# Kernel optimization log

Measured on AMD Instinct MI355X. Metric: run time of the kernel, lower is better.

The kernel has to match this reference:

```python
import jax, jax.numpy as jnp
import numpy as np
from jax import lax

B, T, F, H, L = 64, 2048, 128, 128, 2


def _lstm_layer(x, Wih, Whh, bih, bhh, h0, c0):
    """Single LSTM layer, torch gate order (i,f,g,o). x: [B,T,in] -> y: [B,T,H], hT, cT."""
    b = bih + bhh

    def step(carry, xt):
        h, c = carry
        gates = xt @ Wih.T + h @ Whh.T + b  # [B,4H]
        i, f, g, o = jnp.split(gates, 4, axis=-1)
        i = jax.nn.sigmoid(i)
        f = jax.nn.sigmoid(f)
        g = jnp.tanh(g)
        o = jax.nn.sigmoid(o)
        c = f * c + i * g
        h = o * jnp.tanh(c)
        return (h, c), h

    xs = jnp.swapaxes(x, 0, 1)  # [T,B,in]
    (hT, cT), ys = lax.scan(step, (h0, c0), xs)
    return jnp.swapaxes(ys, 0, 1), hT, cT


def setup_inputs() -> dict:
    key = jax.random.key(0)
    ks = jax.random.split(key, 20)
    s = 1.0 / np.sqrt(H)
    u = lambda k, shape: jax.random.uniform(k, shape, jnp.float32, -s, s)
    inp = {"x": jax.random.normal(ks[0], (B, T, F), jnp.float32)}
    i = 1
    for pre, in0 in (("enc", F), ("dec", H)):
        for l in range(L):
            d_in = in0 if l == 0 else H
            inp[f"{pre}_Wih{l}"] = u(ks[i], (4 * H, d_in)); i += 1
            inp[f"{pre}_Whh{l}"] = u(ks[i], (4 * H, H)); i += 1
            inp[f"{pre}_bih{l}"] = u(ks[i], (4 * H,)); i += 1
            inp[f"{pre}_bhh{l}"] = u(ks[i], (4 * H,)); i += 1
    inp["out_W"] = u(ks[i], (F, H)); i += 1
    inp["out_b"] = u(ks[i], (F,))
    return inp


def reference(x,
              enc_Wih0, enc_Whh0, enc_bih0, enc_bhh0,
              enc_Wih1, enc_Whh1, enc_bih1, enc_bhh1,
              dec_Wih0, dec_Whh0, dec_bih0, dec_bhh0,
              dec_Wih1, dec_Whh1, dec_bih1, dec_bhh1,
              out_W, out_b):
    z = jnp.zeros((x.shape[0], H), x.dtype)
    # encoder: 2 stacked layers, zero initial state
    y0, h0, c0 = _lstm_layer(x, enc_Wih0, enc_Whh0, enc_bih0, enc_bhh0, z, z)
    y1, h1, c1 = _lstm_layer(y0, enc_Wih1, enc_Whh1, enc_bih1, enc_bhh1, z, z)
    # decoder: zeros input, initial state = encoder final (h,c) per layer
    dec_in = jnp.zeros_like(x)  # valid since n_features == hidden_dim
    d0, _, _ = _lstm_layer(dec_in, dec_Wih0, dec_Whh0, dec_bih0, dec_bhh0, h0, c0)
    d1, _, _ = _lstm_layer(d0, dec_Wih1, dec_Whh1, dec_bih1, dec_bhh1, h1, c1)
    return d1 @ out_W.T + out_b
```

## Files before the change

### kernel.cpp

```cpp
#include <hip/hip_runtime.h>
#include <cstdint>
#include <cstddef>

typedef float    float4v __attribute__((ext_vector_type(4)));
typedef _Float16 f16x4   __attribute__((ext_vector_type(4)));
typedef _Float16 f16x8   __attribute__((ext_vector_type(8)));
typedef unsigned long long u64;
struct u64p { u64 a, b; };

#define DI __device__ __forceinline__

static const int Bsz = 64, Tlen = 2048, Hd = 128, G4 = 512;
static const int HSTR = 144;
static const int RING = 256;
static const int YSTR = 136;

DI float sigf_fast(float x) {
    float e = __builtin_amdgcn_exp2f(-1.442695041f * x);
    return __builtin_amdgcn_rcpf(1.f + e);
}
DI float tanhf_fast(float x) {
    float e = __builtin_amdgcn_exp2f(-2.885390082f * x);
    return 2.f * __builtin_amdgcn_rcpf(1.f + e) - 1.f;
}

DI void lds_barrier() {
    asm volatile("s_waitcnt lgkmcnt(0)\n\ts_barrier" ::: "memory");
}

DI void pin(f16x8& v) {
    float4v t = __builtin_bit_cast(float4v, v);
    asm volatile("" : "+v"(t));
    v = __builtin_bit_cast(f16x8, t);
}

DI f16x8 cvt8(const float* p) {
    float4v u = *(const float4v*)p;
    float4v w = *(const float4v*)(p + 4);
    f16x8 o;
    o[0] = (_Float16)u[0]; o[1] = (_Float16)u[1]; o[2] = (_Float16)u[2]; o[3] = (_Float16)u[3];
    o[4] = (_Float16)w[0]; o[5] = (_Float16)w[1]; o[6] = (_Float16)w[2]; o[7] = (_Float16)w[3];
    return o;
}

DI u64 pack4(float4v a) {
    f16x4 h;
    h[0] = (_Float16)a[0]; h[1] = (_Float16)a[1];
    h[2] = (_Float16)a[2]; h[3] = (_Float16)a[3];
    return __builtin_bit_cast(u64, h);
}

DI u64 ald64(const void* pp) {
    return __hip_atomic_load((const u64*)pp, __ATOMIC_RELAXED, __HIP_MEMORY_SCOPE_AGENT);
}
DI void ast64(void* pp, u64 v) {
    __hip_atomic_store((u64*)pp, v, __ATOMIC_RELAXED, __HIP_MEMORY_SCOPE_AGENT);
}
DI void ast16(void* pp, unsigned short v) {
    __hip_atomic_store((unsigned short*)pp, v, __ATOMIC_RELAXED, __HIP_MEMORY_SCOPE_AGENT);
}
DI unsigned int aldu32(const unsigned int* pp) {
    return __hip_atomic_load(pp, __ATOMIC_RELAXED, __HIP_MEMORY_SCOPE_AGENT);
}
DI void astu32(unsigned int* pp, unsigned int v) {
    __hip_atomic_store(pp, v, __ATOMIC_RELAXED, __HIP_MEMORY_SCOPE_AGENT);
}

template <bool P_HAS_XP, bool P_INIT, bool C_INIT, bool R3_OUT>
__global__ __launch_bounds__(512, 1) void lstm_fused5(
    const float* __restrict__ Up, const float* __restrict__ bip, const float* __restrict__ bhp,
    const float* __restrict__ php, const float* __restrict__ pcp,
    float* __restrict__ fhp, float* __restrict__ fcp,
    const float* __restrict__ Wc, const float* __restrict__ Uc,
    const float* __restrict__ bic, const float* __restrict__ bhc,
    const float* __restrict__ phc, const float* __restrict__ pcc,
    float* __restrict__ fhc, float* __restrict__ fcc,
    const float* __restrict__ Wx, const float* __restrict__ xin,
    const float* __restrict__ oW, const float* __restrict__ ob,
    float* __restrict__ outp,
    _Float16* __restrict__ PB,
    _Float16* __restrict__ X2,
    _Float16* __restrict__ X1,
    _Float16* __restrict__ Y1,
    unsigned int* __restrict__ prog,  unsigned int* __restrict__ prog2,
    unsigned int* __restrict__ prog3, unsigned int* __restrict__ prog4,
    unsigned int* __restrict__ prog5, int T)
{
    const int tid  = threadIdx.x;
    const int lane = tid & 63, w = tid >> 6;
    const int col  = lane & 15, quad = lane >> 4;
    const int b    = col & 3, s = col >> 2;
    const int role = blockIdx.x >> 4;
    const int p    = blockIdx.x & 15;
    const int bglob = p * 4 + b;
    const int j    = w * 16 + s * 4 + quad;
    const int NG   = T >> 3;

    __shared__ alignas(16) _Float16 Hl[2 * 4 * HSTR];
    __shared__ alignas(16) _Float16 Ylh[32 * YSTR];

    unsigned int* pr  = prog  + p * 16;
    unsigned int* pr2 = prog2 + p * 16;
    unsigned int* pr3 = P_HAS_XP ? prog3 + p * 16 : nullptr;
    unsigned int* pr4 = R3_OUT   ? prog4 + p * 16 : nullptr;
    unsigned int* pr5 = R3_OUT   ? prog5 + p * 16 : nullptr;

    if (role == 0) {
        f16x8 af[4][4];
#pragma unroll
        for (int mt = 0; mt < 4; mt++) {
            int urow = (col & 3) * 128 + (w * 16 + mt * 4 + (col >> 2));
            const float* ur = Up + (size_t)urow * 128;
#pragma unroll
            for (int kc = 0; kc < 4; kc++) af[mt][kc] = cvt8(ur + kc * 32 + quad * 8);
        }
#pragma unroll
        for (int mt = 0; mt < 4; mt++)
#pragma unroll
            for (int kc = 0; kc < 4; kc++) pin(af[mt][kc]);

        float bq[4];
#pragma unroll
        for (int q = 0; q < 4; q++) bq[q] = bip[q * 128 + j] + bhp[q * 128 + j];

        float c = 0.f, hv = 0.f;
        if (P_INIT) {
            c  = pcp[(size_t)bglob * 128 + j];
            hv = php[(size_t)bglob * 128 + j];
        }
        Hl[b * HSTR + j] = (_Float16)hv;
        __syncthreads();

        const _Float16* x1b = P_HAS_XP ? X1 + (size_t)bglob * RING * 512 + 4 * j : nullptr;
        unsigned short* pbp = (unsigned short*)PB + (size_t)bglob * RING * 128 + j;

        if constexpr (P_HAS_XP) {
            if (tid == 511) {
                unsigned int need = 16u; if (need > (unsigned int)T) need = (unsigned int)T;
                unsigned int psn = aldu32(pr3);
                while (psn < need) { __builtin_amdgcn_s_sleep(8); psn = aldu32(pr3); }
            }
            __syncthreads();
        }
        f16x4 xp = {};
        if (P_HAS_XP) xp = __builtin_bit_cast(f16x4, ald64(x1b));

        int cur = 0;
        for (int g = 0; g < NG; g++) {
#pragma unroll
            for (int k = 0; k < 8; k++) {
                const int t = g * 8 + k;
                f16x4 xpn = {};
                if (P_HAS_XP)
                    xpn = __builtin_bit_cast(f16x4, ald64(x1b + (size_t)((t + 1) & (RING - 1)) * 512));

                const _Float16* Hc = Hl + cur * (4 * HSTR);
                f16x8 bf[4];
#pragma unroll
                for (int kc = 0; kc < 4; kc++)
                    bf[kc] = *(const f16x8*)(Hc + b * HSTR + kc * 32 + quad * 8);

                float4v acc[4] = {};
#pragma unroll
                for (int kc = 0; kc < 4; kc++)
#pragma unroll
                    for (int mt = 0; mt < 4; mt++)
                        acc[mt] = __builtin_amdgcn_mfma_f32_16x16x32_f16(af[mt][kc], bf[kc], acc[mt], 0, 0, 0);

                float4v t0 = (s & 1) ? acc[1] : acc[0];
                float4v t1 = (s & 1) ? acc[3] : acc[2];
                float4v gg = (s & 2) ? t1 : t0;

                float g0 = gg[0] + bq[0], g1 = gg[1] + bq[1], g2 = gg[2] + bq[2], g3 = gg[3] + bq[3];
                if (P_HAS_XP) { g0 += (float)xp[0]; g1 += (float)xp[1]; g2 += (float)xp[2]; g3 += (float)xp[3]; }
                float iv = sigf_fast(g0), fv = sigf_fast(g1);
                float gv = tanhf_fast(g2), ov = sigf_fast(g3);
                c  = fv * c + iv * gv;
                hv = ov * tanhf_fast(c);

                _Float16 hf = (_Float16)hv;
                Hl[(cur ^ 1) * (4 * HSTR) + b * HSTR + j] = hf;
                ast16(pbp + (size_t)(t & (RING - 1)) * 128,
                      __builtin_bit_cast(unsigned short, hf));

                if (k == 7) {
                    if constexpr (P_HAS_XP) asm volatile("s_waitcnt vmcnt(2)" ::: "memory");
                    else                    asm volatile("s_waitcnt vmcnt(1)" ::: "memory");
                    if (tid == 0) astu32(pr, (unsigned int)(g * 8 + 7));
                    if constexpr (P_HAS_XP) {
                        if (tid == 511 && g + 1 < NG) {
                            unsigned int need = (unsigned int)(8 * (g + 1) + 16);
                            if (need > (unsigned int)T) need = (unsigned int)T;
                            unsigned int psn = aldu32(pr3);
                            while (psn < need) { __builtin_amdgcn_s_sleep(2); psn = aldu32(pr3); }
                        }
                    }
                }
                lds_barrier();
                xp = xpn;
                cur ^= 1;
            }
        }

        asm volatile("s_waitcnt vmcnt(0)" ::: "memory");
        __syncthreads();
        if (tid == 0) astu32(pr, (unsigned int)T);

        fhp[(size_t)bglob * 128 + j] = hv;
        fcp[(size_t)bglob * 128 + j] = c;
    } else if (role == 1) {
        f16x8 afH[4][4];
#pragma unroll
        for (int mt = 0; mt < 4; mt++) {
            int urow = (col & 3) * 128 + (w * 16 + mt * 4 + (col >> 2));
            const float* ur = Uc + (size_t)urow * 128;
#pragma unroll
            for (int kc = 0; kc < 4; kc++) afH[mt][kc] = cvt8(ur + kc * 32 + quad * 8);
        }
#pragma unroll
        for (int mt = 0; mt < 4; mt++)
#pragma unroll
            for (int kc = 0; kc < 4; kc++) pin(afH[mt][kc]);

        float bq[4];
#pragma unroll
        for (int q = 0; q < 4; q++) bq[q] = bic[q * 128 + j] + bhc[q * 128 + j];

        float c = 0.f, hv = 0.f;
        if (C_INIT) {
            c  = pcc[(size_t)bglob * 128 + j];
            hv = phc[(size_t)bglob * 128 + j];
        }
        Hl[b * HSTR + j] = (_Float16)hv;

        if (tid == 511) {
            unsigned int need = 9u; if (need > (unsigned int)T) need = (unsigned int)T;
            unsigned int psn = aldu32(pr2);
            while (psn < need) { __builtin_amdgcn_s_sleep(8); psn = aldu32(pr2); }
        }
        __syncthreads();

        const _Float16* x2b = X2 + (size_t)bglob * RING * 512 + 4 * j;
        unsigned short* y1p = R3_OUT ? (unsigned short*)Y1 + (size_t)bglob * RING * 128 + j : nullptr;
        f16x4 xp = __builtin_bit_cast(f16x4, ald64(x2b));

        int cur = 0;
        for (int g = 0; g < NG; g++) {
#pragma unroll
            for (int k = 0; k < 8; k++) {
                const int t = g * 8 + k;
                const int slot = (t + 1) & (RING - 1);
                f16x4 xpn = __builtin_bit_cast(f16x4, ald64(x2b + (size_t)slot * 512));

                const _Float16* Hc = Hl + cur * (4 * HSTR);
                f16x8 bf[4];
#pragma unroll
                for (int kc = 0; kc < 4; kc++)
                    bf[kc] = *(const f16x8*)(Hc + b * HSTR + kc * 32 + quad * 8);

                float4v acc[4] = {};
#pragma unroll
                for (int kc = 0; kc < 4; kc++)
#pragma unroll
                    for (int mt = 0; mt < 4; mt++)
                        acc[mt] = __builtin_amdgcn_mfma_f32_16x16x32_f16(afH[mt][kc], bf[kc], acc[mt], 0, 0, 0);

                float4v t0 = (s & 1) ? acc[1] : acc[0];
                float4v t1 = (s & 1) ? acc[3] : acc[2];
                float4v gg = (s & 2) ? t1 : t0;

                float g0 = gg[0] + bq[0] + (float)xp[0], g1 = gg[1] + bq[1] + (float)xp[1];
                float g2 = gg[2] + bq[2] + (float)xp[2], g3 = gg[3] + bq[3] + (float)xp[3];
                float iv = sigf_fast(g0), fv = sigf_fast(g1);
                float gv = tanhf_fast(g2), ov = sigf_fast(g3);
                c  = fv * c + iv * gv;
                hv = ov * tanhf_fast(c);

                _Float16 hf = (_Float16)hv;
                Hl[(cur ^ 1) * (4 * HSTR) + b * HSTR + j] = hf;
                if constexpr (R3_OUT)
                    ast16(y1p + (size_t)(t & (RING - 1)) * 128,
                          __builtin_bit_cast(unsigned short, hf));

                if (k == 7) {
                    if constexpr (R3_OUT) {
                        asm volatile("s_waitcnt vmcnt(2)" ::: "memory");
                        if (tid == 0) astu32(pr4, (unsigned int)(g * 8 + 7));
                    }
                    if (tid == 511 && g + 1 < NG) {
                        unsigned int need = (unsigned int)(8 * (g + 1) + 9);
                        if (need > (unsigned int)T) need = (unsigned int)T;
                        unsigned int psn = aldu32(pr2);
                        while (psn < need) { __builtin_amdgcn_s_sleep(2); psn = aldu32(pr2); }
                        if constexpr (R3_OUT) {
                            if (g + 1 >= 32) {
                                unsigned int need5 = (unsigned int)(8 * (g + 1 - 32) + 8);
                                unsigned int p5 = aldu32(pr5);
                                while (p5 < need5) { __builtin_amdgcn_s_sleep(2); p5 = aldu32(pr5); }
                            }
                        }
                    }
                }
                lds_barrier();
                xp = xpn;
                cur ^= 1;
            }
        }

        if constexpr (R3_OUT) {
            asm volatile("s_waitcnt vmcnt(0)" ::: "memory");
            __syncthreads();
            if (tid == 0) astu32(pr4, (unsigned int)T);
        }
        fhc[(size_t)bglob * 128 + j] = hv;
        fcc[(size_t)bglob * 128 + j] = c;
    } else if (role == 2) {
        f16x8 bw[4][4];
#pragma unroll
        for (int nt = 0; nt < 4; nt++) {
            int n = (w * 4 + nt) * 16 + col;
            int wrow = (n & 3) * 128 + (n >> 2);
            const float* Wr = Wc + (size_t)wrow * 128;
#pragma unroll
            for (int kc = 0; kc < 4; kc++) bw[nt][kc] = cvt8(Wr + kc * 32 + quad * 8);
        }
#pragma unroll
        for (int nt = 0; nt < 4; nt++)
#pragma unroll
            for (int kc = 0; kc < 4; kc++) pin(bw[nt][kc]);

        const int lrow = tid >> 4, lchunk = tid & 15;
        const int lb = lrow & 3, ltr = lrow >> 2;

        for (int g = 0; g < NG; g++) {
            if (tid == 0) {
                unsigned int need = (unsigned int)(g * 8 + 8);
                unsigned int psn = aldu32(pr);
                while (psn < need) { __builtin_amdgcn_s_sleep(4); psn = aldu32(pr); }
            }
            __syncthreads();
            {
                int slot = (g * 8 + ltr) & (RING - 1);
                const char* srcp = (const char*)(PB + ((size_t)(p * 4 + lb) * RING + slot) * 128 + lchunk * 8);
                u64 a0 = ald64(srcp);
                u64 a1 = ald64(srcp + 8);
                char* dst = (char*)&Ylh[lrow * YSTR + lchunk * 8];
                *(u64*)dst = a0;
                *(u64*)(dst + 8) = a1;
            }
            lds_barrier();

            float4v acc[2][4] = {};
#pragma unroll
            for (int kc = 0; kc < 4; kc++) {
                f16x8 y0 = *(const f16x8*)&Ylh[col * YSTR + kc * 32 + quad * 8];
                f16x8 y1t = *(const f16x8*)&Ylh[(16 + col) * YSTR + kc * 32 + quad * 8];
#pragma unroll
                for (int nt = 0; nt < 4; nt++) {
                    acc[0][nt] = __builtin_amdgcn_mfma_f32_16x16x32_f16(bw[nt][kc], y0,  acc[0][nt], 0, 0, 0);
                    acc[1][nt] = __builtin_amdgcn_mfma_f32_16x16x32_f16(bw[nt][kc], y1t, acc[1][nt], 0, 0, 0);
                }
            }
            {
                const int bb = col & 3;
#pragma unroll
                for (int mt = 0; mt < 2; mt++) {
                    int trow = mt * 4 + (col >> 2);
                    int slot = (g * 8 + trow) & (RING - 1);
                    _Float16* dst = X2 + ((size_t)(p * 4 + bb) * RING + slot) * 512 + (w * 4) * 16 + quad * 4;
#pragma unroll
                    for (int nt = 0; nt < 4; nt++)
                        ast64(dst + nt * 16, pack4(acc[mt][nt]));
                }
            }
            asm volatile("s_waitcnt vmcnt(0)" ::: "memory");
            __syncthreads();
            if (tid == 0) astu32(pr2, (unsigned int)(g * 8 + 8));
        }
    } else if constexpr (!R3_OUT) {
        f16x8 bw[4][4];
#pragma unroll
        for (int nt = 0; nt < 4; nt++) {
            int n = (w * 4 + nt) * 16 + col;
            int wrow = (n & 3) * 128 + (n >> 2);
            const float* Wr = Wx + (size_t)wrow * 128;
#pragma unroll
            for (int kc = 0; kc < 4; kc++) bw[nt][kc] = cvt8(Wr + kc * 32 + quad * 8);
        }
#pragma unroll
        for (int nt = 0; nt < 4; nt++)
#pragma unroll
            for (int kc = 0; kc < 4; kc++) pin(bw[nt][kc]);

        const int lrow = tid >> 4, lchunk = tid & 15;
        const int lb = lrow & 3, ltr = lrow >> 2;
        const float* xsrc = xin + (size_t)(p * 4 + lb) * T * 128 + lchunk * 8;

        for (int g = 0; g < NG; g++) {
            if (g >= 32 && tid == 0) {
                unsigned int need = (unsigned int)(8 * (g - 32));
                unsigned int psn = aldu32(pr);
                while (psn < need) { __builtin_amdgcn_s_sleep(4); psn = aldu32(pr); }
            }
            __syncthreads();
            {
                f16x8 xv = cvt8(xsrc + (size_t)(g * 8 + ltr) * 128);
                u64p w2 = __builtin_bit_cast(u64p, xv);
                char* dst = (char*)&Ylh[lrow * YSTR + lchunk * 8];
                *(u64*)dst = w2.a;
                *(u64*)(dst + 8) = w2.b;
            }
            lds_barrier();

            float4v acc[2][4] = {};
#pragma unroll
            for (int kc = 0; kc < 4; kc++) {
                f16x8 y0 = *(const f16x8*)&Ylh[col * YSTR + kc * 32 + quad * 8];
                f16x8 y1t = *(const f16x8*)&Ylh[(16 + col) * YSTR + kc * 32 + quad * 8];
#pragma unroll
                for (int nt = 0; nt < 4; nt++) {
                    acc[0][nt] = __builtin_amdgcn_mfma_f32_16x16x32_f16(bw[nt][kc], y0,  acc[0][nt], 0, 0, 0);
                    acc[1][nt] = __builtin_amdgcn_mfma_f32_16x16x32_f16(bw[nt][kc], y1t, acc[1][nt], 0, 0, 0);
                }
            }
            {
                const int bb = col & 3;
#pragma unroll
                for (int mt = 0; mt < 2; mt++) {
                    int trow = mt * 4 + (col >> 2);
                    int slot = (g * 8 + trow) & (RING - 1);
                    _Float16* dst = X1 + ((size_t)(p * 4 + bb) * RING + slot) * 512 + (w * 4) * 16 + quad * 4;
#pragma unroll
                    for (int nt = 0; nt < 4; nt++)
                        ast64(dst + nt * 16, pack4(acc[mt][nt]));
                }
            }
            asm volatile("s_waitcnt vmcnt(0)" ::: "memory");
            __syncthreads();
            if (tid == 0) astu32(pr3, (unsigned int)(g * 8 + 8));
        }
    } else {
        f16x8 bo[4];
#pragma unroll
        for (int kc = 0; kc < 4; kc++) bo[kc] = cvt8(oW + (size_t)(w * 16 + col) * 128 + kc * 32 + quad * 8);
#pragma unroll
        for (int kc = 0; kc < 4; kc++) pin(bo[kc]);
        float4v bv4 = *(const float4v*)(ob + w * 16 + quad * 4);

        const int lrow = tid >> 4, lchunk = tid & 15;
        const int lb = lrow & 3, ltr = lrow >> 2;

        for (int g = 0; g < NG; g++) {
            if (tid == 0) {
                unsigned int need = (unsigned int)(g * 8 + 8);
                unsigned int psn = aldu32(pr4);
                while (psn < need) { __builtin_amdgcn_s_sleep(4); psn = aldu32(pr4); }
            }
            __syncthreads();
            {
                int slot = (g * 8 + ltr) & (RING - 1);
                const char* srcp = (const char*)(Y1 + ((size_t)(p * 4 + lb) * RING + slot) * 128 + lchunk * 8);
                u64 a0 = ald64(srcp);
                u64 a1 = ald64(srcp + 8);
                char* dst = (char*)&Ylh[lrow * YSTR + lchunk * 8];
                *(u64*)dst = a0;
                *(u64*)(dst + 8) = a1;
            }
            lds_barrier();
            if (tid == 0) astu32(pr5, (unsigned int)(g * 8 + 8));

            float4v acc[2] = {};
#pragma unroll
            for (int kc = 0; kc < 4; kc++) {
                f16x8 y0 = *(const f16x8*)&Ylh[col * YSTR + kc * 32 + quad * 8];
                f16x8 y1t = *(const f16x8*)&Ylh[(16 + col) * YSTR + kc * 32 + quad * 8];
                acc[0] = __builtin_amdgcn_mfma_f32_16x16x32_f16(bo[kc], y0,  acc[0], 0, 0, 0);
                acc[1] = __builtin_amdgcn_mfma_f32_16x16x32_f16(bo[kc], y1t, acc[1], 0, 0, 0);
            }
            {
                const int bb = col & 3;
#pragma unroll
                for (int mt = 0; mt < 2; mt++) {
                    int trow = mt * 4 + (col >> 2);
                    float4v v = acc[mt];
                    v[0] += bv4[0]; v[1] += bv4[1]; v[2] += bv4[2]; v[3] += bv4[3];
                    *(float4v*)(outp + ((size_t)(p * 4 + bb) * T + g * 8 + trow) * 128 + w * 16 + quad * 4) = v;
                }
            }
        }
    }
}

extern "C" void kernel_launch(void* const* d_in, const int* in_sizes, int n_in,
                              void* d_out, int out_size, void* d_ws, size_t ws_size,
                              hipStream_t stream)
{
    const float* x    = (const float*)d_in[0];
    const float* eW0  = (const float*)d_in[1];
    const float* eU0  = (const float*)d_in[2];
    const float* eb0i = (const float*)d_in[3];
    const float* eb0h = (const float*)d_in[4];
    const float* eW1  = (const float*)d_in[5];
    const float* eU1  = (const float*)d_in[6];
    const float* eb1i = (const float*)d_in[7];
    const float* eb1h = (const float*)d_in[8];
    const float* dU0  = (const float*)d_in[10];
    const float* db0i = (const float*)d_in[11];
    const float* db0h = (const float*)d_in[12];
    const float* dW1  = (const float*)d_in[13];
    const float* dU1  = (const float*)d_in[14];
    const float* db1i = (const float*)d_in[15];
    const float* db1h = (const float*)d_in[16];
    const float* oW   = (const float*)d_in[17];
    const float* ob   = (const float*)d_in[18];

    char* ws = (char*)d_ws;
    _Float16* X1  = (_Float16*)(ws);
    _Float16* X2A = (_Float16*)(ws + (16u << 20));
    _Float16* PBA = (_Float16*)(ws + (32u << 20));
    _Float16* X2B = (_Float16*)(ws + (36u << 20));
    _Float16* PBB = (_Float16*)(ws + (52u << 20));
    _Float16* Y1R = (_Float16*)(ws + (56u << 20));
    float*    fh0 = (float*)(ws + (88u << 20));
    float*    fc0 = fh0 + Bsz * Hd;
    float*    fh1 = fc0 + Bsz * Hd;
    float*    fc1 = fh1 + Bsz * Hd;
    unsigned int* pg = (unsigned int*)(ws + (88u << 20) + (1u << 17));
    unsigned int* progA  = pg + 0 * 256;
    unsigned int* prog2A = pg + 1 * 256;
    unsigned int* prog3A = pg + 2 * 256;
    unsigned int* progB  = pg + 3 * 256;
    unsigned int* prog2B = pg + 4 * 256;
    unsigned int* prog4B = pg + 5 * 256;
    unsigned int* prog5B = pg + 6 * 256;

    hipMemsetAsync((void*)pg, 0, 8192, stream);

    lstm_fused5<true, false, false, false><<<dim3(64), dim3(512), 0, stream>>>(
        eU0, eb0i, eb0h, (const float*)nullptr, (const float*)nullptr, fh0, fc0,
        eW1, eU1, eb1i, eb1h, (const float*)nullptr, (const float*)nullptr, fh1, fc1,
        eW0, x,
        (const float*)nullptr, (const float*)nullptr, (float*)nullptr,
        PBA, X2A, X1, (_Float16*)nullptr,
        progA, prog2A, prog3A, (unsigned int*)nullptr, (unsigned int*)nullptr, Tlen);

    lstm_fused5<false, true, true, true><<<dim3(64), dim3(512), 0, stream>>>(
        dU0, db0i, db0h, fh0, fc0, fh0, fc0,
        dW1, dU1, db1i, db1h, fh1, fc1, fh1, fc1,
        (const float*)nullptr, (const float*)nullptr,
        oW, ob, (float*)d_out,
        PBB, X2B, (_Float16*)nullptr, Y1R,
        progB, prog2B, (unsigned int*)nullptr, prog4B, prog5B, Tlen);
}
```

Baseline: 2.576 ms.

## Merge encoder and decoder LSTM kernels into one persistent megakernel

Fuses the two launches (encoder and decoder) into a single 80-block persistent kernel. Each recurrent role runs 2T steps, swapping to decoder weights at the midpoint while keeping h and c in registers, which removes the global final-state round trip. The output projection blocks run alongside and start as soon as decoder rows appear. Progress-counter polls are also prefetched one group ahead to hide flag-load latency. This removes the launch gap and the pipeline fill and drain between phases, at the cost of running more blocks at once and a more complex dependency chain.

```diff
diff --git a/kernel.cpp b/kernel.cpp
--- a/kernel.cpp
+++ b/kernel.cpp
@@ -10,7 +10,7 @@
 
 #define DI __device__ __forceinline__
 
-static const int Bsz = 64, Tlen = 2048, Hd = 128, G4 = 512;
+static const int Bsz = 64, Tlen = 2048, Hd = 128;
 static const int HSTR = 144;
 static const int RING = 256;
 static const int YSTR = 136;
@@ -66,17 +66,14 @@
     __hip_atomic_store(pp, v, __ATOMIC_RELAXED, __HIP_MEMORY_SCOPE_AGENT);
 }
 
-template <bool P_HAS_XP, bool P_INIT, bool C_INIT, bool R3_OUT>
-__global__ __launch_bounds__(512, 1) void lstm_fused5(
-    const float* __restrict__ Up, const float* __restrict__ bip, const float* __restrict__ bhp,
-    const float* __restrict__ php, const float* __restrict__ pcp,
-    float* __restrict__ fhp, float* __restrict__ fcp,
-    const float* __restrict__ Wc, const float* __restrict__ Uc,
-    const float* __restrict__ bic, const float* __restrict__ bhc,
-    const float* __restrict__ phc, const float* __restrict__ pcc,
-    float* __restrict__ fhc, float* __restrict__ fcc,
-    const float* __restrict__ Wx, const float* __restrict__ xin,
-    const float* __restrict__ oW, const float* __restrict__ ob,
+__global__ __launch_bounds__(512, 1) void lstm_mega(
+    const float* __restrict__ eU0, const float* __restrict__ eb0i, const float* __restrict__ eb0h,
+    const float* __restrict__ dU0, const float* __restrict__ db0i, const float* __restrict__ db0h,
+    const float* __restrict__ eU1, const float* __restrict__ eb1i, const float* __restrict__ eb1h,
+    const float* __restrict__ dU1, const float* __restrict__ db1i, const float* __restrict__ db1h,
+    const float* __restrict__ eW1, const float* __restrict__ dW1,
+    const float* __restrict__ eW0, const float* __restrict__ xin,
+    const float* __restrict__ oW,  const float* __restrict__ ob,
     float* __restrict__ outp,
     _Float16* __restrict__ PB,
     _Float16* __restrict__ X2,
@@ -95,244 +92,332 @@
     const int bglob = p * 4 + b;
     const int j    = w * 16 + s * 4 + quad;
     const int NG   = T >> 3;
+    const int NG2  = NG * 2;
+    const unsigned int T2 = (unsigned int)(2 * T);
 
     __shared__ alignas(16) _Float16 Hl[2 * 4 * HSTR];
     __shared__ alignas(16) _Float16 Ylh[32 * YSTR];
 
     unsigned int* pr  = prog  + p * 16;
     unsigned int* pr2 = prog2 + p * 16;
-    unsigned int* pr3 = P_HAS_XP ? prog3 + p * 16 : nullptr;
-    unsigned int* pr4 = R3_OUT   ? prog4 + p * 16 : nullptr;
-    unsigned int* pr5 = R3_OUT   ? prog5 + p * 16 : nullptr;
+    unsigned int* pr3 = prog3 + p * 16;
+    unsigned int* pr4 = prog4 + p * 16;
+    unsigned int* pr5 = prog5 + p * 16;
 
     if (role == 0) {
         f16x8 af[4][4];
+        float bq[4];
 #pragma unroll
         for (int mt = 0; mt < 4; mt++) {
             int urow = (col & 3) * 128 + (w * 16 + mt * 4 + (col >> 2));
-            const float* ur = Up + (size_t)urow * 128;
-#pragma unroll
-            for (int kc = 0; kc < 4; kc++) af[mt][kc] = cvt8(ur + kc * 32 + quad * 8);
-        }
-#pragma unroll
-        for (int mt = 0; mt < 4; mt++)
-#pragma unroll
-            for (int kc = 0; kc < 4; kc++) pin(af[mt][kc]);
-
-        float bq[4];
-#pragma unroll
-        for (int q = 0; q < 4; q++) bq[q] = bip[q * 128 + j] + bhp[q * 128 + j];
+            const float* ur = eU0 + (size_t)urow * 128;
+#pragma unroll
+            for (int kc = 0; kc < 4; kc++) { af[mt][kc] = cvt8(ur + kc * 32 + quad * 8); pin(af[mt][kc]); }
+        }
+#pragma unroll
+        for (int q = 0; q < 4; q++) bq[q] = eb0i[q * 128 + j] + eb0h[q * 128 + j];
 
         float c = 0.f, hv = 0.f;
-        if (P_INIT) {
-            c  = pcp[(size_t)bglob * 128 + j];
-            hv = php[(size_t)bglob * 128 + j];
-        }
-        Hl[b * HSTR + j] = (_Float16)hv;
+        Hl[b * HSTR + j] = (_Float16)0.f;
         __syncthreads();
 
-        const _Float16* x1b = P_HAS_XP ? X1 + (size_t)bglob * RING * 512 + 4 * j : nullptr;
+        const _Float16* x1b = X1 + (size_t)bglob * RING * 512 + 4 * j;
         unsigned short* pbp = (unsigned short*)PB + (size_t)bglob * RING * 128 + j;
 
-        if constexpr (P_HAS_XP) {
-            if (tid == 511) {
-                unsigned int need = 16u; if (need > (unsigned int)T) need = (unsigned int)T;
-                unsigned int psn = aldu32(pr3);
-                while (psn < need) { __builtin_amdgcn_s_sleep(8); psn = aldu32(pr3); }
-            }
-            __syncthreads();
-        }
-        f16x4 xp = {};
-        if (P_HAS_XP) xp = __builtin_bit_cast(f16x4, ald64(x1b));
+        if (tid == 511) {
+            unsigned int need = 16u; if (need > (unsigned int)T) need = (unsigned int)T;
+            unsigned int psn = aldu32(pr3);
+            while (psn < need) { __builtin_amdgcn_s_sleep(8); psn = aldu32(pr3); }
+        }
+        __syncthreads();
+        f16x4 xp = __builtin_bit_cast(f16x4, ald64(x1b));
 
         int cur = 0;
-        for (int g = 0; g < NG; g++) {
-#pragma unroll
-            for (int k = 0; k < 8; k++) {
-                const int t = g * 8 + k;
-                f16x4 xpn = {};
-                if (P_HAS_XP)
-                    xpn = __builtin_bit_cast(f16x4, ald64(x1b + (size_t)((t + 1) & (RING - 1)) * 512));
-
-                const _Float16* Hc = Hl + cur * (4 * HSTR);
-                f16x8 bf[4];
-#pragma unroll
-                for (int kc = 0; kc < 4; kc++)
-                    bf[kc] = *(const f16x8*)(Hc + b * HSTR + kc * 32 + quad * 8);
-
-                float4v acc[4] = {};
-#pragma unroll
-                for (int kc = 0; kc < 4; kc++)
-#pragma unroll
-                    for (int mt = 0; mt < 4; mt++)
-                        acc[mt] = __builtin_amdgcn_mfma_f32_16x16x32_f16(af[mt][kc], bf[kc], acc[mt], 0, 0, 0);
-
-                float4v t0 = (s & 1) ? acc[1] : acc[0];
-                float4v t1 = (s & 1) ? acc[3] : acc[2];
-                float4v gg = (s & 2) ? t1 : t0;
-
-                float g0 = gg[0] + bq[0], g1 = gg[1] + bq[1], g2 = gg[2] + bq[2], g3 = gg[3] + bq[3];
-                if (P_HAS_XP) { g0 += (float)xp[0]; g1 += (float)xp[1]; g2 += (float)xp[2]; g3 += (float)xp[3]; }
-                float iv = sigf_fast(g0), fv = sigf_fast(g1);
-                float gv = tanhf_fast(g2), ov = sigf_fast(g3);
-                c  = fv * c + iv * gv;
-                hv = ov * tanhf_fast(c);
-
-                _Float16 hf = (_Float16)hv;
-                Hl[(cur ^ 1) * (4 * HSTR) + b * HSTR + j] = hf;
-                ast16(pbp + (size_t)(t & (RING - 1)) * 128,
-                      __builtin_bit_cast(unsigned short, hf));
-
-                if (k == 7) {
-                    if constexpr (P_HAS_XP) asm volatile("s_waitcnt vmcnt(2)" ::: "memory");
-                    else                    asm volatile("s_waitcnt vmcnt(1)" ::: "memory");
-                    if (tid == 0) astu32(pr, (unsigned int)(g * 8 + 7));
-                    if constexpr (P_HAS_XP) {
+        unsigned int pf3 = 0, ps3 = 0;
+        for (int g = 0; g < NG2; g++) {
+            if (g == NG) {
+#pragma unroll
+                for (int mt = 0; mt < 4; mt++) {
+                    int urow = (col & 3) * 128 + (w * 16 + mt * 4 + (col >> 2));
+                    const float* ur = dU0 + (size_t)urow * 128;
+#pragma unroll
+                    for (int kc = 0; kc < 4; kc++) { af[mt][kc] = cvt8(ur + kc * 32 + quad * 8); pin(af[mt][kc]); }
+                }
+#pragma unroll
+                for (int q = 0; q < 4; q++) bq[q] = db0i[q * 128 + j] + db0h[q * 128 + j];
+            }
+            if (g < NG) {
+                if (tid == 511 && g + 1 < NG) pf3 = aldu32(pr3);
+#pragma unroll
+                for (int k = 0; k < 8; k++) {
+                    const int t = g * 8 + k;
+                    f16x4 xpn = __builtin_bit_cast(f16x4,
+                        ald64(x1b + (size_t)((t + 1) & (RING - 1)) * 512));
+
+                    const _Float16* Hc = Hl + cur * (4 * HSTR);
+                    f16x8 bf[4];
+#pragma unroll
+                    for (int kc = 0; kc < 4; kc++)
+                        bf[kc] = *(const f16x8*)(Hc + b * HSTR + kc * 32 + quad * 8);
+
+                    float4v acc[4] = {};
+#pragma unroll
+                    for (int kc = 0; kc < 4; kc++)
+#pragma unroll
+                        for (int mt = 0; mt < 4; mt++)
+                            acc[mt] = __builtin_amdgcn_mfma_f32_16x16x32_f16(af[mt][kc], bf[kc], acc[mt], 0, 0, 0);
+
+                    float4v t0 = (s & 1) ? acc[1] : acc[0];
+                    float4v t1 = (s & 1) ? acc[3] : acc[2];
+                    float4v gg = (s & 2) ? t1 : t0;
+
+                    float g0 = gg[0] + bq[0] + (float)xp[0], g1 = gg[1] + bq[1] + (float)xp[1];
+                    float g2 = gg[2] + bq[2] + (float)xp[2], g3 = gg[3] + bq[3] + (float)xp[3];
+                    float iv = sigf_fast(g0), fv = sigf_fast(g1);
+                    float gv = tanhf_fast(g2), ov = sigf_fast(g3);
+                    c  = fv * c + iv * gv;
+                    hv = ov * tanhf_fast(c);
+
+                    _Float16 hf = (_Float16)hv;
+                    Hl[(cur ^ 1) * (4 * HSTR) + b * HSTR + j] = hf;
+                    ast16(pbp + (size_t)(t & (RING - 1)) * 128,
+                          __builtin_bit_cast(unsigned short, hf));
+
+                    if (k == 7) {
+                        asm volatile("s_waitcnt vmcnt(2)" ::: "memory");
+                        if (tid == 0) astu32(pr, (unsigned int)(g * 8 + 7));
                         if (tid == 511 && g + 1 < NG) {
                             unsigned int need = (unsigned int)(8 * (g + 1) + 16);
                             if (need > (unsigned int)T) need = (unsigned int)T;
-                            unsigned int psn = aldu32(pr3);
-                            while (psn < need) { __builtin_amdgcn_s_sleep(2); psn = aldu32(pr3); }
+                            if (ps3 < pf3) ps3 = pf3;
+                            while (ps3 < need) { __builtin_amdgcn_s_sleep(2); ps3 = aldu32(pr3); }
                         }
                     }
-                }
-                lds_barrier();
-                xp = xpn;
-                cur ^= 1;
-            }
-        }
-
+                    lds_barrier();
+                    xp = xpn;
+                    cur ^= 1;
+                }
+            } else {
+#pragma unroll
+                for (int k = 0; k < 8; k++) {
+                    const int t = g * 8 + k;
+
+                    const _Float16* Hc = Hl + cur * (4 * HSTR);
+                    f16x8 bf[4];
+#pragma unroll
+                    for (int kc = 0; kc < 4; kc++)
+                        bf[kc] = *(const f16x8*)(Hc + b * HSTR + kc * 32 + quad * 8);
+
+                    float4v acc[4] = {};
+#pragma unroll
+                    for (int kc = 0; kc < 4; kc++)
+#pragma unroll
+                        for (int mt = 0; mt < 4; mt++)
+                            acc[mt] = __builtin_amdgcn_mfma_f32_16x16x32_f16(af[mt][kc], bf[kc], acc[mt], 0, 0, 0);
+
+                    float4v t0 = (s & 1) ? acc[1] : acc[0];
+                    float4v t1 = (s & 1) ? acc[3] : acc[2];
+                    float4v gg = (s & 2) ? t1 : t0;
+
+                    float g0 = gg[0] + bq[0], g1 = gg[1] + bq[1];
+                    float g2 = gg[2] + bq[2], g3 = gg[3] + bq[3];
+                    float iv = sigf_fast(g0), fv = sigf_fast(g1);
+                    float gv = tanhf_fast(g2), ov = sigf_fast(g3);
+                    c  = fv * c + iv * gv;
+                    hv = ov * tanhf_fast(c);
+
+                    _Float16 hf = (_Float16)hv;
+                    Hl[(cur ^ 1) * (4 * HSTR) + b * HSTR + j] = hf;
+                    ast16(pbp + (size_t)(t & (RING - 1)) * 128,
+                          __builtin_bit_cast(unsigned short, hf));
+
+                    if (k == 7) {
+                        asm volatile("s_waitcnt vmcnt(1)" ::: "memory");
+                        if (tid == 0) astu32(pr, (unsigned int)(g * 8 + 7));
+                    }
+                    lds_barrier();
+                    cur ^= 1;
+                }
+            }
+        }
         asm volatile("s_waitcnt vmcnt(0)" ::: "memory");
         __syncthreads();
-        if (tid == 0) astu32(pr, (unsigned int)T);
-
-        fhp[(size_t)bglob * 128 + j] = hv;
-        fcp[(size_t)bglob * 128 + j] = c;
+        if (tid == 0) astu32(pr, T2);
     } else if (role == 1) {
         f16x8 afH[4][4];
+        float bq[4];
 #pragma unroll
         for (int mt = 0; mt < 4; mt++) {
             int urow = (col & 3) * 128 + (w * 16 + mt * 4 + (col >> 2));
-            const float* ur = Uc + (size_t)urow * 128;
-#pragma unroll
-            for (int kc = 0; kc < 4; kc++) afH[mt][kc] = cvt8(ur + kc * 32 + quad * 8);
-        }
-#pragma unroll
-        for (int mt = 0; mt < 4; mt++)
-#pragma unroll
-            for (int kc = 0; kc < 4; kc++) pin(afH[mt][kc]);
-
-        float bq[4];
-#pragma unroll
-        for (int q = 0; q < 4; q++) bq[q] = bic[q * 128 + j] + bhc[q * 128 + j];
+            const float* ur = eU1 + (size_t)urow * 128;
+#pragma unroll
+            for (int kc = 0; kc < 4; kc++) { afH[mt][kc] = cvt8(ur + kc * 32 + quad * 8); pin(afH[mt][kc]); }
+        }
+#pragma unroll
+        for (int q = 0; q < 4; q++) bq[q] = eb1i[q * 128 + j] + eb1h[q * 128 + j];
 
         float c = 0.f, hv = 0.f;
-        if (C_INIT) {
-            c  = pcc[(size_t)bglob * 128 + j];
-            hv = phc[(size_t)bglob * 128 + j];
-        }
-        Hl[b * HSTR + j] = (_Float16)hv;
+        Hl[b * HSTR + j] = (_Float16)0.f;
 
         if (tid == 511) {
-            unsigned int need = 9u; if (need > (unsigned int)T) need = (unsigned int)T;
+            unsigned int need = 9u; if (need > T2) need = T2;
             unsigned int psn = aldu32(pr2);
             while (psn < need) { __builtin_amdgcn_s_sleep(8); psn = aldu32(pr2); }
         }
         __syncthreads();
 
         const _Float16* x2b = X2 + (size_t)bglob * RING * 512 + 4 * j;
-        unsigned short* y1p = R3_OUT ? (unsigned short*)Y1 + (size_t)bglob * RING * 128 + j : nullptr;
+        unsigned short* y1p = (unsigned short*)Y1 + (size_t)bglob * RING * 128 + j;
         f16x4 xp = __builtin_bit_cast(f16x4, ald64(x2b));
 
         int cur = 0;
-        for (int g = 0; g < NG; g++) {
-#pragma unroll
-            for (int k = 0; k < 8; k++) {
-                const int t = g * 8 + k;
-                const int slot = (t + 1) & (RING - 1);
-                f16x4 xpn = __builtin_bit_cast(f16x4, ald64(x2b + (size_t)slot * 512));
-
-                const _Float16* Hc = Hl + cur * (4 * HSTR);
-                f16x8 bf[4];
-#pragma unroll
-                for (int kc = 0; kc < 4; kc++)
-                    bf[kc] = *(const f16x8*)(Hc + b * HSTR + kc * 32 + quad * 8);
-
-                float4v acc[4] = {};
-#pragma unroll
-                for (int kc = 0; kc < 4; kc++)
-#pragma unroll
-                    for (int mt = 0; mt < 4; mt++)
-                        acc[mt] = __builtin_amdgcn_mfma_f32_16x16x32_f16(afH[mt][kc], bf[kc], acc[mt], 0, 0, 0);
-
-                float4v t0 = (s & 1) ? acc[1] : acc[0];
-                float4v t1 = (s & 1) ? acc[3] : acc[2];
-                float4v gg = (s & 2) ? t1 : t0;
-
-                float g0 = gg[0] + bq[0] + (float)xp[0], g1 = gg[1] + bq[1] + (float)xp[1];
-                float g2 = gg[2] + bq[2] + (float)xp[2], g3 = gg[3] + bq[3] + (float)xp[3];
-                float iv = sigf_fast(g0), fv = sigf_fast(g1);
-                float gv = tanhf_fast(g2), ov = sigf_fast(g3);
-                c  = fv * c + iv * gv;
-                hv = ov * tanhf_fast(c);
-
-                _Float16 hf = (_Float16)hv;
-                Hl[(cur ^ 1) * (4 * HSTR) + b * HSTR + j] = hf;
-                if constexpr (R3_OUT)
+        unsigned int pf2 = 0, ps2 = 0, pf5 = 0, ps5 = 0;
+        for (int g = 0; g < NG2; g++) {
+            if (g == NG) {
+#pragma unroll
+                for (int mt = 0; mt < 4; mt++) {
+                    int urow = (col & 3) * 128 + (w * 16 + mt * 4 + (col >> 2));
+                    const float* ur = dU1 + (size_t)urow * 128;
+#pragma unroll
+                    for (int kc = 0; kc < 4; kc++) { afH[mt][kc] = cvt8(ur + kc * 32 + quad * 8); pin(afH[mt][kc]); }
+                }
+#pragma unroll
+                for (int q = 0; q < 4; q++) bq[q] = db1i[q * 128 + j] + db1h[q * 128 + j];
+            }
+            if (tid == 511) {
+                if (g + 1 < NG2) pf2 = aldu32(pr2);
+                if (g + 1 >= NG + 32 && g + 1 < NG2) pf5 = aldu32(pr5);
+            }
+            if (g < NG) {
+#pragma unroll
+                for (int k = 0; k < 8; k++) {
+                    const int t = g * 8 + k;
+                    f16x4 xpn = __builtin_bit_cast(f16x4,
+                        ald64(x2b + (size_t)((t + 1) & (RING - 1)) * 512));
+
+                    const _Float16* Hc = Hl + cur * (4 * HSTR);
+                    f16x8 bf[4];
+#pragma unroll
+                    for (int kc = 0; kc < 4; kc++)
+                        bf[kc] = *(const f16x8*)(Hc + b * HSTR + kc * 32 + quad * 8);
+
+                    float4v acc[4] = {};
+#pragma unroll
+                    for (int kc = 0; kc < 4; kc++)
+#pragma unroll
+                        for (int mt = 0; mt < 4; mt++)
+                            acc[mt] = __builtin_amdgcn_mfma_f32_16x16x32_f16(afH[mt][kc], bf[kc], acc[mt], 0, 0, 0);
+
+                    float4v t0 = (s & 1) ? acc[1] : acc[0];
+                    float4v t1 = (s & 1) ? acc[3] : acc[2];
+                    float4v gg = (s & 2) ? t1 : t0;
+
+                    float g0 = gg[0] + bq[0] + (float)xp[0], g1 = gg[1] + bq[1] + (float)xp[1];
+                    float g2 = gg[2] + bq[2] + (float)xp[2], g3 = gg[3] + bq[3] + (float)xp[3];
+                    float iv = sigf_fast(g0), fv = sigf_fast(g1);
+                    float gv = tanhf_fast(g2), ov = sigf_fast(g3);
+                    c  = fv * c + iv * gv;
+                    hv = ov * tanhf_fast(c);
+
+                    Hl[(cur ^ 1) * (4 * HSTR) + b * HSTR + j] = (_Float16)hv;
+
+                    if (k == 7) {
+                        if (tid == 511 && g + 1 < NG2) {
+                            unsigned int need = (unsigned int)(8 * (g + 1) + 9);
+                            if (need > T2) need = T2;
+                            if (ps2 < pf2) ps2 = pf2;
+                            while (ps2 < need) { __builtin_amdgcn_s_sleep(2); ps2 = aldu32(pr2); }
+                        }
+                    }
+                    lds_barrier();
+                    xp = xpn;
+                    cur ^= 1;
+                }
+            } else {
+#pragma unroll
+                for (int k = 0; k < 8; k++) {
+                    const int t = g * 8 + k;
+                    f16x4 xpn = __builtin_bit_cast(f16x4,
+                        ald64(x2b + (size_t)((t + 1) & (RING - 1)) * 512));
+
+                    const _Float16* Hc = Hl + cur * (4 * HSTR);
+                    f16x8 bf[4];
+#pragma unroll
+                    for (int kc = 0; kc < 4; kc++)
+                        bf[kc] = *(const f16x8*)(Hc + b * HSTR + kc * 32 + quad * 8);
+
+                    float4v acc[4] = {};
+#pragma unroll
+                    for (int kc = 0; kc < 4; kc++)
+#pragma unroll
+                        for (int mt = 0; mt < 4; mt++)
+                            acc[mt] = __builtin_amdgcn_mfma_f32_16x16x32_f16(afH[mt][kc], bf[kc], acc[mt], 0, 0, 0);
+
+                    float4v t0 = (s & 1) ? acc[1] : acc[0];
+                    float4v t1 = (s & 1) ? acc[3] : acc[2];
+                    float4v gg = (s & 2) ? t1 : t0;
+
+                    float g0 = gg[0] + bq[0] + (float)xp[0], g1 = gg[1] + bq[1] + (float)xp[1];
+                    float g2 = gg[2] + bq[2] + (float)xp[2], g3 = gg[3] + bq[3] + (float)xp[3];
+                    float iv = sigf_fast(g0), fv = sigf_fast(g1);
+                    float gv = tanhf_fast(g2), ov = sigf_fast(g3);
+                    c  = fv * c + iv * gv;
+                    hv = ov * tanhf_fast(c);
+
+                    _Float16 hf = (_Float16)hv;
+                    Hl[(cur ^ 1) * (4 * HSTR) + b * HSTR + j] = hf;
                     ast16(y1p + (size_t)(t & (RING - 1)) * 128,
                           __builtin_bit_cast(unsigned short, hf));
 
-                if (k == 7) {
-                    if constexpr (R3_OUT) {
+                    if (k == 7) {
                         asm volatile("s_waitcnt vmcnt(2)" ::: "memory");
                         if (tid == 0) astu32(pr4, (unsigned int)(g * 8 + 7));
-                    }
-                    if (tid == 511 && g + 1 < NG) {
-                        unsigned int need = (unsigned int)(8 * (g + 1) + 9);
-                        if (need > (unsigned int)T) need = (unsigned int)T;
-                        unsigned int psn = aldu32(pr2);
-                        while (psn < need) { __builtin_amdgcn_s_sleep(2); psn = aldu32(pr2); }
-                        if constexpr (R3_OUT) {
-                            if (g + 1 >= 32) {
+                        if (tid == 511 && g + 1 < NG2) {
+                            unsigned int need = (unsigned int)(8 * (g + 1) + 9);
+                            if (need > T2) need = T2;
+                            if (ps2 < pf2) ps2 = pf2;
+                            while (ps2 < need) { __builtin_amdgcn_s_sleep(2); ps2 = aldu32(pr2); }
+                            if (g + 1 >= NG + 32) {
                                 unsigned int need5 = (unsigned int)(8 * (g + 1 - 32) + 8);
-                                unsigned int p5 = aldu32(pr5);
-                                while (p5 < need5) { __builtin_amdgcn_s_sleep(2); p5 = aldu32(pr5); }
+                                if (ps5 < pf5) ps5 = pf5;
+                                while (ps5 < need5) { __builtin_amdgcn_s_sleep(2); ps5 = aldu32(pr5); }
                             }
                         }
                     }
-                }
-                lds_barrier();
-                xp = xpn;
-                cur ^= 1;
-            }
-        }
-
-        if constexpr (R3_OUT) {
-            asm volatile("s_waitcnt vmcnt(0)" ::: "memory");
-            __syncthreads();
-            if (tid == 0) astu32(pr4, (unsigned int)T);
-        }
-        fhc[(size_t)bglob * 128 + j] = hv;
-        fcc[(size_t)bglob * 128 + j] = c;
+                    lds_barrier();
+                    xp = xpn;
+                    cur ^= 1;
+                }
+            }
+        }
+        asm volatile("s_waitcnt vmcnt(0)" ::: "memory");
+        __syncthreads();
+        if (tid == 0) astu32(pr4, T2);
     } else if (role == 2) {
         f16x8 bw[4][4];
 #pragma unroll
         for (int nt = 0; nt < 4; nt++) {
             int n = (w * 4 + nt) * 16 + col;
             int wrow = (n & 3) * 128 + (n >> 2);
-            const float* Wr = Wc + (size_t)wrow * 128;
-#pragma unroll
-            for (int kc = 0; kc < 4; kc++) bw[nt][kc] = cvt8(Wr + kc * 32 + quad * 8);
-        }
-#pragma unroll
-        for (int nt = 0; nt < 4; nt++)
-#pragma unroll
-            for (int kc = 0; kc < 4; kc++) pin(bw[nt][kc]);
+            const float* Wr = eW1 + (size_t)wrow * 128;
+#pragma unroll
+            for (int kc = 0; kc < 4; kc++) { bw[nt][kc] = cvt8(Wr + kc * 32 + quad * 8); pin(bw[nt][kc]); }
+        }
 
         const int lrow = tid >> 4, lchunk = tid & 15;
         const int lb = lrow & 3, ltr = lrow >> 2;
 
-        for (int g = 0; g < NG; g++) {
+        for (int g = 0; g < NG2; g++) {
+            if (g == NG) {
+#pragma unroll
+                for (int nt = 0; nt < 4; nt++) {
+                    int n = (w * 4 + nt) * 16 + col;
+                    int wrow = (n & 3) * 128 + (n >> 2);
+                    const float* Wr = dW1 + (size_t)wrow * 128;
+#pragma unroll
+                    for (int kc = 0; kc < 4; kc++) { bw[nt][kc] = cvt8(Wr + kc * 32 + quad * 8); pin(bw[nt][kc]); }
+                }
+            }
             if (tid == 0) {
                 unsigned int need = (unsigned int)(g * 8 + 8);
                 unsigned int psn = aldu32(pr);
@@ -377,20 +462,16 @@
             __syncthreads();
             if (tid == 0) astu32(pr2, (unsigned int)(g * 8 + 8));
         }
-    } else if constexpr (!R3_OUT) {
+    } else if (role == 3) {
         f16x8 bw[4][4];
 #pragma unroll
         for (int nt = 0; nt < 4; nt++) {
             int n = (w * 4 + nt) * 16 + col;
             int wrow = (n & 3) * 128 + (n >> 2);
-            const float* Wr = Wx + (size_t)wrow * 128;
-#pragma unroll
-            for (int kc = 0; kc < 4; kc++) bw[nt][kc] = cvt8(Wr + kc * 32 + quad * 8);
-        }
-#pragma unroll
-        for (int nt = 0; nt < 4; nt++)
-#pragma unroll
-            for (int kc = 0; kc < 4; kc++) pin(bw[nt][kc]);
+            const float* Wr = eW0 + (size_t)wrow * 128;
+#pragma unroll
+            for (int kc = 0; kc < 4; kc++) { bw[nt][kc] = cvt8(Wr + kc * 32 + quad * 8); pin(bw[nt][kc]); }
+        }
 
         const int lrow = tid >> 4, lchunk = tid & 15;
         const int lb = lrow & 3, ltr = lrow >> 2;
@@ -442,15 +523,14 @@
     } else {
         f16x8 bo[4];
 #pragma unroll
-        for (int kc = 0; kc < 4; kc++) bo[kc] = cvt8(oW + (size_t)(w * 16 + col) * 128 + kc * 32 + quad * 8);
-#pragma unroll
-        for (int kc = 0; kc < 4; kc++) pin(bo[kc]);
+        for (int kc = 0; kc < 4; kc++) { bo[kc] = cvt8(oW + (size_t)(w * 16 + col) * 128 + kc * 32 + quad * 8); pin(bo[kc]); }
         float4v bv4 = *(const float4v*)(ob + w * 16 + quad * 4);
 
         const int lrow = tid >> 4, lchunk = tid & 15;
         const int lb = lrow & 3, ltr = lrow >> 2;
 
-        for (int g = 0; g < NG; g++) {
+        for (int gg = 0; gg < NG; gg++) {
+            const int g = NG + gg;
             if (tid == 0) {
                 unsigned int need = (unsigned int)(g * 8 + 8);
                 unsigned int psn = aldu32(pr4);
@@ -484,7 +564,7 @@
                     int trow = mt * 4 + (col >> 2);
                     float4v v = acc[mt];
                     v[0] += bv4[0]; v[1] += bv4[1]; v[2] += bv4[2]; v[3] += bv4[3];
-                    *(float4v*)(outp + ((size_t)(p * 4 + bb) * T + g * 8 + trow) * 128 + w * 16 + quad * 4) = v;
+                    *(float4v*)(outp + ((size_t)(p * 4 + bb) * T + gg * 8 + trow) * 128 + w * 16 + quad * 4) = v;
                 }
             }
         }
@@ -515,40 +595,18 @@
     const float* ob   = (const float*)d_in[18];
 
     char* ws = (char*)d_ws;
-    _Float16* X1  = (_Float16*)(ws);
-    _Float16* X2A = (_Float16*)(ws + (16u << 20));
-    _Float16* PBA = (_Float16*)(ws + (32u << 20));
-    _Float16* X2B = (_Float16*)(ws + (36u << 20));
-    _Float16* PBB = (_Float16*)(ws + (52u << 20));
-    _Float16* Y1R = (_Float16*)(ws + (56u << 20));
-    float*    fh0 = (float*)(ws + (88u << 20));
-    float*    fc0 = fh0 + Bsz * Hd;
-    float*    fh1 = fc0 + Bsz * Hd;
-    float*    fc1 = fh1 + Bsz * Hd;
-    unsigned int* pg = (unsigned int*)(ws + (88u << 20) + (1u << 17));
-    unsigned int* progA  = pg + 0 * 256;
-    unsigned int* prog2A = pg + 1 * 256;
-    unsigned int* prog3A = pg + 2 * 256;
-    unsigned int* progB  = pg + 3 * 256;
-    unsigned int* prog2B = pg + 4 * 256;
-    unsigned int* prog4B = pg + 5 * 256;
-    unsigned int* prog5B = pg + 6 * 256;
+    _Float16* X1 = (_Float16*)(ws);
+    _Float16* X2 = (_Float16*)(ws + (16u << 20));
+    _Float16* PB = (_Float16*)(ws + (32u << 20));
+    _Float16* Y1 = (_Float16*)(ws + (36u << 20));
+    unsigned int* pg = (unsigned int*)(ws + (40u << 20));
 
     hipMemsetAsync((void*)pg, 0, 8192, stream);
 
-    lstm_fused5<true, false, false, false><<<dim3(64), dim3(512), 0, stream>>>(
-        eU0, eb0i, eb0h, (const float*)nullptr, (const float*)nullptr, fh0, fc0,
-        eW1, eU1, eb1i, eb1h, (const float*)nullptr, (const float*)nullptr, fh1, fc1,
-        eW0, x,
-        (const float*)nullptr, (const float*)nullptr, (float*)nullptr,
-        PBA, X2A, X1, (_Float16*)nullptr,
-        progA, prog2A, prog3A, (unsigned int*)nullptr, (unsigned int*)nullptr, Tlen);
-
-    lstm_fused5<false, true, true, true><<<dim3(64), dim3(512), 0, stream>>>(
-        dU0, db0i, db0h, fh0, fc0, fh0, fc0,
-        dW1, dU1, db1i, db1h, fh1, fc1, fh1, fc1,
-        (const float*)nullptr, (const float*)nullptr,
-        oW, ob, (float*)d_out,
-        PBB, X2B, (_Float16*)nullptr, Y1R,
-        progB, prog2B, (unsigned int*)nullptr, prog4B, prog5B, Tlen);
-}
+    lstm_mega<<<dim3(80), dim3(512), 0, stream>>>(
+        eU0, eb0i, eb0h, dU0, db0i, db0h,
+        eU1, eb1i, eb1h, dU1, db1i, db1h,
+        eW1, dW1, eW0, x, oW, ob, (float*)d_out,
+        PB, X2, X1, Y1,
+        pg, pg + 256, pg + 512, pg + 768, pg + 1024, Tlen);
+}
```

Result: faster. 2.400 ms (-6.8%).
